# Kernel optimization log

Hardware: AMD Instinct MI355X
Metric: run time of the kernel (lower is better)

The kernel has to match this reference:

```python
import jax, jax.numpy as jnp
import numpy as np

B, C, H, W = 16, 512, 32, 32
GROUPS = 8
EPS = 1e-5


def setup_inputs() -> dict:
    key = jax.random.key(0)
    ks = jax.random.split(key, 7)
    s = 1.0 / np.sqrt(C)
    return {
        "x": jax.random.normal(ks[0], (B, C, H, W), dtype=jnp.float32),
        "gamma": jnp.ones((C,), dtype=jnp.float32),
        "beta": jnp.zeros((C,), dtype=jnp.float32),
        "w_qkv": jax.random.normal(ks[1], (3 * C, C), dtype=jnp.float32) * s,
        "b_qkv": jnp.zeros((3 * C,), dtype=jnp.float32),
        "w_proj": jax.random.normal(ks[2], (C, C), dtype=jnp.float32) * s,
        "b_proj": jnp.zeros((C,), dtype=jnp.float32),
    }


def group_norm(x, gamma, beta):
    b, c, h, w = x.shape
    xg = x.reshape(b, GROUPS, c // GROUPS, h, w)
    mean = xg.mean(axis=(2, 3, 4), keepdims=True)
    var = xg.var(axis=(2, 3, 4), keepdims=True)
    xn = ((xg - mean) * jax.lax.rsqrt(var + EPS)).reshape(b, c, h, w)
    return xn * gamma[None, :, None, None] + beta[None, :, None, None]


def reference(x, gamma, beta, w_qkv, b_qkv, w_proj, b_proj):
    b, c, h, w = x.shape
    n = h * w
    hn = group_norm(x, gamma, beta)
    # 1x1 conv == channel matmul: [3C, C] x [B, C, N] -> [B, 3C, N]
    qkv = jnp.einsum('oc,bcn->bon', w_qkv, hn.reshape(b, c, n)) + b_qkv[None, :, None]
    q, k, v = jnp.split(qkv, 3, axis=1)  # each [B, C, N]
    scale = c ** (-0.5)
    # scores [B, N, N]: q^T k
    attn = jax.nn.softmax(jnp.einsum('bcn,bcm->bnm', q, k) * scale, axis=-1)
    out = jnp.einsum('bnm,bcm->bcn', attn, v)  # [B, C, N]
    proj = jnp.einsum('oc,bcn->bon', w_proj, out) + b_proj[None, :, None]
    return x + proj.reshape(b, c, h, w)
```

## Files before the change

kernel.cpp:

```cpp
#include <hip/hip_runtime.h>


#define BATCH 16
#define CCH 512
#define NSP 1024
#define EPSV 1e-5f
#define BK 32
#define HT 4096

typedef short bf16x8 __attribute__((ext_vector_type(8)));
typedef float f32x4 __attribute__((ext_vector_type(4)));

__device__ __forceinline__ unsigned short f2bf(float f) {
    unsigned int u = __float_as_uint(f);
    u += 0x7FFF + ((u >> 16) & 1);
    return (unsigned short)(u >> 16);
}

__device__ __forceinline__ void glds16(const void* g, void* l) {
    __builtin_amdgcn_global_load_lds(
        (const __attribute__((address_space(1))) unsigned int*)g,
        (__attribute__((address_space(3))) unsigned int*)l, 16, 0, 0);
}

#define XCD_MAP(GX_LOG2, PER, xv, yv, bv)                 \
    const int lin_ = blockIdx.x;                          \
    const int xcd_ = lin_ & 7;                            \
    int slot_ = lin_ >> 3;                                \
    const int hi_ = (slot_ >= (PER)) ? 1 : 0;             \
    const int bv = xcd_ + 8 * hi_;                        \
    slot_ -= hi_ * (PER);                                 \
    const int xv = slot_ & ((1 << (GX_LOG2)) - 1);        \
    const int yv = slot_ >> (GX_LOG2);

__device__ __forceinline__ void gemm128_loop(
    const unsigned short* __restrict__ Ag, const unsigned short* __restrict__ Bg,
    int astr, int bstr, int ktot, short* Al, short* Bl, f32x4* acc) {
    const int t = threadIdx.x;
    const int w = t >> 6, lane = t & 63;
    const int wr = (w >> 1) * 64, wc = (w & 1) * 64;
    const int fr = lane & 15;
    const int fsw = (((lane >> 4) ^ (fr & 3)) * 8);
    const int r0 = t >> 2;
    const int kc = (((t & 3) ^ (r0 & 3)) * 8);
    const unsigned short* Ap0 = Ag + (size_t)r0 * astr + kc;
    const unsigned short* Ap1 = Ag + (size_t)(r0 + 64) * astr + kc;
    const unsigned short* Bp0 = Bg + (size_t)r0 * bstr + kc;
    const unsigned short* Bp1 = Bg + (size_t)(r0 + 64) * bstr + kc;
    short* Alw = Al + w * 512;
    short* Blw = Bl + w * 512;
    for (int k0 = 0; k0 < ktot; k0 += 64) {
        glds16(Ap0 + k0, Alw);
        glds16(Ap1 + k0, Alw + 2048);
        glds16(Ap0 + k0 + 32, Alw + HT);
        glds16(Ap1 + k0 + 32, Alw + HT + 2048);
        glds16(Bp0 + k0, Blw);
        glds16(Bp1 + k0, Blw + 2048);
        glds16(Bp0 + k0 + 32, Blw + HT);
        glds16(Bp1 + k0 + 32, Blw + HT + 2048);
        __syncthreads();
#pragma unroll
        for (int h = 0; h < 2; h++) {
            const short* Ab = Al + h * HT;
            const short* Bb = Bl + h * HT;
            bf16x8 af[4], bfr[4];
#pragma unroll
            for (int mi = 0; mi < 4; mi++)
                af[mi] = *(const bf16x8*)(Ab + (wr + mi * 16 + fr) * BK + fsw);
#pragma unroll
            for (int ni = 0; ni < 4; ni++)
                bfr[ni] = *(const bf16x8*)(Bb + (wc + ni * 16 + fr) * BK + fsw);
#pragma unroll
            for (int mi = 0; mi < 4; mi++)
#pragma unroll
                for (int ni = 0; ni < 4; ni++)
                    acc[mi * 4 + ni] = __builtin_amdgcn_mfma_f32_16x16x32_bf16(
                        af[mi], bfr[ni], acc[mi * 4 + ni], 0, 0, 0);
        }
        __syncthreads();
    }
}

#define EPI_SETUP()                                          \
    const int t = threadIdx.x, lane = t & 63, w = t >> 6;    \
    const int wr = (w >> 1) * 64, wc = (w & 1) * 64;         \
    const int fr = lane & 15, rr0 = (lane >> 4) * 4;

#define ACC_INIT(acc)                                        \
    f32x4 acc[16];                                           \
    _Pragma("unroll") for (int i = 0; i < 16; i++)           \
        acc[i] = (f32x4){0.f, 0.f, 0.f, 0.f};

__global__ __launch_bounds__(256) void setup_k(
    const float* __restrict__ x, float* __restrict__ stats,
    const float* __restrict__ wa, unsigned short* __restrict__ oa, int na4,
    const float* __restrict__ wb, unsigned short* __restrict__ ob, int nb4,
    float* __restrict__ Lsum, const float* __restrict__ bqv,
    unsigned short* __restrict__ wv_t, float* __restrict__ puv) {
    const int t = threadIdx.x;
    const int bx = blockIdx.x;
    __shared__ float rs[4], rq[4];
    __shared__ __align__(16) unsigned short Tt[64 * 72];
    if (bx < 128) {
        const int bg = bx;
        const float4* xp = (const float4*)(x + (size_t)bg * 65536);
        float s = 0.f, q = 0.f;
#pragma unroll
        for (int i = 0; i < 64; i++) {
            float4 v = xp[t + i * 256];
            s += v.x + v.y + v.z + v.w;
            q += v.x * v.x + v.y * v.y + v.z * v.z + v.w * v.w;
        }
#pragma unroll
        for (int off = 32; off; off >>= 1) {
            s += __shfl_down(s, off);
            q += __shfl_down(q, off);
        }
        const int wave = t >> 6, lane = t & 63;
        if (lane == 0) { rs[wave] = s; rq[wave] = q; }
        __syncthreads();
        if (t == 0) {
            float S = rs[0] + rs[1] + rs[2] + rs[3];
            float Q = rq[0] + rq[1] + rq[2] + rq[3];
            const float inv = 1.f / 65536.f;
            float mean = S * inv;
            float var = Q * inv - mean * mean;
            stats[bg * 2] = mean;
            stats[bg * 2 + 1] = rsqrtf(var + EPSV);
        }
    } else if (bx < 896) {
        int i = (bx - 128) * 256 + t;
        const float* src;
        unsigned short* dst;
        int j;
        if (i < na4) { src = wa; dst = oa; j = i; }
        else { j = i - na4; if (j >= nb4) return; src = wb; dst = ob; }
        float4 v = ((const float4*)src)[j];
        ushort4 o;
        o.x = f2bf(v.x); o.y = f2bf(v.y); o.z = f2bf(v.z); o.w = f2bf(v.w);
        ((ushort4*)dst)[j] = o;
    } else if (bx < 912) {
        int i = (bx - 896) * 256 + t;
        ((float4*)Lsum)[i] = (float4){0.f, 0.f, 0.f, 0.f};
    } else if (bx < 976) {
        const int r = bx - 912;
        const float* src = wa + (size_t)2 * 512 * 512;
        const int to = (r >> 3) * 64, tc = (r & 7) * 64;
        const int ol = t >> 2, cs = t & 3;
#pragma unroll
        for (int j = 0; j < 4; j++) {
            float4 v = *(const float4*)(src + (size_t)(to + ol) * 512 + tc + cs * 16 + j * 4);
            int c = cs * 16 + j * 4;
            Tt[(c + 0) * 72 + ol] = f2bf(v.x);
            Tt[(c + 1) * 72 + ol] = f2bf(v.y);
            Tt[(c + 2) * 72 + ol] = f2bf(v.z);
            Tt[(c + 3) * 72 + ol] = f2bf(v.w);
        }
        __syncthreads();
        const int cl = t >> 2, os = t & 3;
        unsigned short* d = wv_t + (size_t)(tc + cl) * 512 + to + os * 16;
        const unsigned short* s2 = Tt + cl * 72 + os * 16;
        *(uint4*)d = *(const uint4*)s2;
        *(uint4*)(d + 8) = *(const uint4*)(s2 + 8);
    } else {
        const int o = (bx - 976) * 256 + t;
        const float* wr_ = wb + (size_t)o * 512;
        const float* bv = bqv + 1024;
        float s = 0.f;
        for (int vv = 0; vv < 512; vv += 4) {
            s += wr_[vv] * bv[vv] + wr_[vv + 1] * bv[vv + 1]
               + wr_[vv + 2] * bv[vv + 2] + wr_[vv + 3] * bv[vv + 3];
        }
        puv[o] = s;
    }
}

__global__ __launch_bounds__(256) void gn_tr_k(
    const float* __restrict__ x, const float* __restrict__ gamma,
    const float* __restrict__ beta, const float* __restrict__ stats,
    unsigned short* __restrict__ hn_t,
    const unsigned short* __restrict__ wp_bf, const unsigned short* __restrict__ wv_t,
    unsigned short* __restrict__ wpv_bf) {
    __shared__ __align__(16) short SM[4 * HT];
    const int lin = blockIdx.x;
    const int t = threadIdx.x;
    if (lin < 16) {
        const int ot = (lin >> 2) * 128, ct2 = (lin & 3) * 128;
        ACC_INIT(acc);
        gemm128_loop(wp_bf + (size_t)ot * 512, wv_t + (size_t)ct2 * 512,
                     512, 512, 512, SM, SM + 2 * HT, acc);
        EPI_SETUP();
#pragma unroll
        for (int ni = 0; ni < 4; ni++) {
            int col = ct2 + wc + ni * 16 + fr;
#pragma unroll
            for (int mi = 0; mi < 4; mi++) {
                int row = ot + wr + mi * 16 + rr0;
#pragma unroll
                for (int r = 0; r < 4; r++)
                    wpv_bf[(size_t)(row + r) * 512 + col] = f2bf(acc[mi * 4 + ni][r]);
            }
        }
        return;
    }
    const int l2 = lin - 16;
    const int nt = l2 & 15, ct = (l2 >> 4) & 7, b = l2 >> 7;
    unsigned short* T = (unsigned short*)SM;
    const float mean = stats[(b * 8 + ct) * 2];
    const float rstd = stats[(b * 8 + ct) * 2 + 1];
    const int cl = t >> 2, nc = t & 3;
    const int c = ct * 64 + cl;
    const float ga = gamma[c] * rstd;
    const float be = beta[c] - mean * ga;
    const float4* xp = (const float4*)(x + ((size_t)b * CCH + c) * NSP + nt * 64);
#pragma unroll
    for (int j = 0; j < 4; j++) {
        float4 v = xp[nc * 4 + j];
        int n = nc * 16 + j * 4;
        T[(n + 0) * 72 + cl] = f2bf(v.x * ga + be);
        T[(n + 1) * 72 + cl] = f2bf(v.y * ga + be);
        T[(n + 2) * 72 + cl] = f2bf(v.z * ga + be);
        T[(n + 3) * 72 + cl] = f2bf(v.w * ga + be);
    }
    __syncthreads();
    const int nl = t >> 2, cc = t & 3;
    unsigned short* dst = hn_t + ((size_t)b * NSP + nt * 64 + nl) * CCH + ct * 64 + cc * 16;
    const unsigned short* src = T + nl * 72 + cc * 16;
    *(uint4*)dst = *(const uint4*)src;
    *(uint4*)(dst + 8) = *(const uint4*)(src + 8);
}

__global__ __launch_bounds__(256) void gemm_qku_k(
    const unsigned short* __restrict__ hn_t, const unsigned short* __restrict__ wq,
    const float* __restrict__ bq, const unsigned short* __restrict__ wpv_bf,
    const float* __restrict__ puv, unsigned short* __restrict__ QKt,
    unsigned short* __restrict__ Ub) {
    __shared__ __align__(16) short Al[2 * HT], Bl[2 * HT];
    XCD_MAP(3, 96, xb, y, b);
    const int ntc = xb * 128;
    ACC_INIT(acc);
    if (y < 8) {
        const int mt = y * 128;
        gemm128_loop(hn_t + ((size_t)b * NSP + mt) * CCH,
                     wq + (size_t)ntc * CCH, CCH, CCH, CCH, Al, Bl, acc);
        unsigned short* Ob = QKt + (size_t)b * NSP * 1024;
        EPI_SETUP();
#pragma unroll
        for (int ni = 0; ni < 4; ni++) {
            int col = ntc + wc + ni * 16 + fr;
            float bias = bq[col];
#pragma unroll
            for (int mi = 0; mi < 4; mi++) {
                int row = mt + wr + mi * 16 + rr0;
#pragma unroll
                for (int r = 0; r < 4; r++)
                    Ob[(size_t)(row + r) * 1024 + col] = f2bf(acc[mi * 4 + ni][r] + bias);
            }
        }
    } else {
        const int mt = (y - 8) * 128;
        gemm128_loop(wpv_bf + (size_t)mt * 512,
                     hn_t + ((size_t)b * NSP + ntc) * CCH, 512, CCH, 512, Al, Bl, acc);
        unsigned short* Ob = Ub + (size_t)b * CCH * NSP;
        EPI_SETUP();
#pragma unroll
        for (int mi = 0; mi < 4; mi++) {
            int row = mt + wr + mi * 16 + rr0;
#pragma unroll
            for (int r = 0; r < 4; r++) {
                float bias = puv[row + r];
#pragma unroll
                for (int ni = 0; ni < 4; ni++) {
                    int col = ntc + wc + ni * 16 + fr;
                    Ob[(size_t)(row + r) * NSP + col] = f2bf(acc[mi * 4 + ni][r] + bias);
                }
            }
        }
    }
}

__global__ __launch_bounds__(256) void gemm_scores_k(
    const unsigned short* __restrict__ QKt, unsigned short* __restrict__ expS,
    float* __restrict__ Lsum) {
    __shared__ __align__(16) short Al[2 * HT], Bl[2 * HT];
    XCD_MAP(3, 64, xb, yb, b);
    const int nt = xb * 128, mt = yb * 128;
    const unsigned short* base = QKt + (size_t)b * NSP * 1024;
    ACC_INIT(acc);
    gemm128_loop(base + (size_t)mt * 1024, base + (size_t)nt * 1024 + 512,
                 1024, 1024, 512, Al, Bl, acc);
    unsigned short* Ob = expS + (size_t)b * NSP * NSP;
    float* Ls = Lsum + (size_t)b * NSP;
    const float scale = 0.044194173824159216f;
    EPI_SETUP();
#pragma unroll
    for (int mi = 0; mi < 4; mi++) {
#pragma unroll
        for (int r = 0; r < 4; r++) {
            const int row = mt + wr + mi * 16 + rr0 + r;
            float rs = 0.f;
#pragma unroll
            for (int ni = 0; ni < 4; ni++) {
                int col = nt + wc + ni * 16 + fr;
                float e = __expf(acc[mi * 4 + ni][r] * scale);
                Ob[(size_t)row * NSP + col] = f2bf(e);
                rs += e;
            }
            rs += __shfl_xor(rs, 1);
            rs += __shfl_xor(rs, 2);
            rs += __shfl_xor(rs, 4);
            rs += __shfl_xor(rs, 8);
            if (fr == 0) atomicAdd(&Ls[row], rs);
        }
    }
}

__global__ __launch_bounds__(256) void gemm_pu_k(
    const unsigned short* __restrict__ Ub, const unsigned short* __restrict__ expS,
    const float* __restrict__ Lsum, const float* __restrict__ x,
    const float* __restrict__ bp, float* __restrict__ out) {
    __shared__ __align__(16) short Al[2 * HT], Bl[2 * HT];
    XCD_MAP(3, 32, xb, yb, b);
    const int nt = xb * 128, ot = yb * 128;
    ACC_INIT(acc);
    gemm128_loop(Ub + ((size_t)b * CCH + ot) * NSP,
                 expS + ((size_t)b * NSP + nt) * NSP, NSP, NSP, NSP, Al, Bl, acc);
    const float* Ls = Lsum + (size_t)b * NSP;
    const size_t bbase = (size_t)b * CCH * NSP;
    EPI_SETUP();
#pragma unroll
    for (int ni = 0; ni < 4; ni++) {
        int col = nt + wc + ni * 16 + fr;
        float invl = __builtin_amdgcn_rcpf(Ls[col]);
#pragma unroll
        for (int mi = 0; mi < 4; mi++) {
            int row = ot + wr + mi * 16 + rr0;
#pragma unroll
            for (int r = 0; r < 4; r++) {
                size_t idx = bbase + (size_t)(row + r) * NSP + col;
                out[idx] = x[idx] + bp[row + r] + acc[mi * 4 + ni][r] * invl;
            }
        }
    }
}

extern "C" void kernel_launch(void* const* d_in, const int* in_sizes, int n_in,
                              void* d_out, int out_size, void* d_ws, size_t ws_size,
                              hipStream_t stream) {
    const float* x = (const float*)d_in[0];
    const float* gamma = (const float*)d_in[1];
    const float* beta = (const float*)d_in[2];
    const float* w_qkv = (const float*)d_in[3];
    const float* b_qkv = (const float*)d_in[4];
    const float* w_proj = (const float*)d_in[5];
    const float* b_proj = (const float*)d_in[6];
    float* out = (float*)d_out;

    char* ws = (char*)d_ws;
    const size_t MB = 1048576;
    const size_t KB = 1024;
    unsigned short* wqkv_bf = (unsigned short*)ws;
    unsigned short* wproj_bf = (unsigned short*)(ws + 1572864);
    float* stats = (float*)(ws + 2 * MB);
    float* Lsum = (float*)(ws + 2 * MB + 64 * KB);
    float* puv = (float*)(ws + 2 * MB + 128 * KB);
    unsigned short* wv_t = (unsigned short*)(ws + 2 * MB + 256 * KB);
    unsigned short* wpv_bf = (unsigned short*)(ws + 3 * MB);
    unsigned short* hn_t = (unsigned short*)(ws + 4 * MB);
    unsigned short* QKt = (unsigned short*)(ws + 24 * MB);
    unsigned short* Ub = (unsigned short*)(ws + 60 * MB);
    unsigned short* expS = (unsigned short*)(ws + 80 * MB);

    setup_k<<<978, 256, 0, stream>>>(x, stats, w_qkv, wqkv_bf, 131072,
                                     w_proj, wproj_bf, 65536, Lsum, b_qkv,
                                     wv_t, puv);
    gn_tr_k<<<2064, 256, 0, stream>>>(x, gamma, beta, stats, hn_t,
                                      wproj_bf, wv_t, wpv_bf);
    gemm_qku_k<<<1536, 256, 0, stream>>>(hn_t, wqkv_bf, b_qkv, wpv_bf, puv,
                                         QKt, Ub);
    gemm_scores_k<<<1024, 256, 0, stream>>>(QKt, expS, Lsum);
    gemm_pu_k<<<512, 256, 0, stream>>>(Ub, expS, Lsum, x, b_proj, out);
}
```

Before: 221.0 us.

## Double-buffer LDS staging in GEMM kernels to overlap loads with MFMA

Adds a double-buffered GEMM main loop that issues global-to-LDS loads for the next 64-wide K slab while computing on the current one, synchronized with explicit vmcnt waits and barriers. The QK/U, scores and PU GEMM kernels switch to it, doubling their LDS footprint to 64 KB per block. The fused weight-product path keeps the single-buffered loop. The aim is to hide global load latency behind MFMA work, at the cost of LDS occupancy and a wasted trailing prefetch that wraps to K offset 0.

New measurement: 204.6 us (median of 3 runs). 1.08x faster.

```diff
diff --git a/kernel.cpp b/kernel.cpp
--- a/kernel.cpp
+++ b/kernel.cpp
@@ -22,6 +22,9 @@
         (const __attribute__((address_space(1))) unsigned int*)g,
         (__attribute__((address_space(3))) unsigned int*)l, 16, 0, 0);
 }
+
+#define MEMF asm volatile("" ::: "memory")
+#define VMW(n) asm volatile("s_waitcnt vmcnt(" #n ")" ::: "memory")
 
 #define XCD_MAP(GX_LOG2, PER, xv, yv, bv)                 \
     const int lin_ = blockIdx.x;                          \
@@ -33,7 +36,75 @@
     const int xv = slot_ & ((1 << (GX_LOG2)) - 1);        \
     const int yv = slot_ >> (GX_LOG2);
 
-__device__ __forceinline__ void gemm128_loop(
+__device__ __forceinline__ void gemm128_dbuf(
+    const unsigned short* __restrict__ Ag, const unsigned short* __restrict__ Bg,
+    int astr, int bstr, int ktot, short* L, f32x4* acc) {
+    const int t = threadIdx.x;
+    const int w = t >> 6, lane = t & 63;
+    const int wr = (w >> 1) * 64, wc = (w & 1) * 64;
+    const int fr = lane & 15;
+    const int fsw = (((lane >> 4) ^ (fr & 3)) * 8);
+    const int r0 = t >> 2;
+    const int kc = (((t & 3) ^ (r0 & 3)) * 8);
+    const unsigned short* Ap0 = Ag + (size_t)r0 * astr + kc;
+    const unsigned short* Ap1 = Ag + (size_t)(r0 + 64) * astr + kc;
+    const unsigned short* Bp0 = Bg + (size_t)r0 * bstr + kc;
+    const unsigned short* Bp1 = Bg + (size_t)(r0 + 64) * bstr + kc;
+    short* lw = L + w * 512;
+
+#define STG(bf, kk) do {                                  \
+    short* aw_ = lw + (bf) * (4 * HT);                    \
+    short* bw_ = aw_ + 2 * HT;                            \
+    glds16(Ap0 + (kk), aw_);                              \
+    glds16(Ap1 + (kk), aw_ + 2048);                       \
+    glds16(Ap0 + (kk) + 32, aw_ + HT);                    \
+    glds16(Ap1 + (kk) + 32, aw_ + HT + 2048);             \
+    glds16(Bp0 + (kk), bw_);                              \
+    glds16(Bp1 + (kk), bw_ + 2048);                       \
+    glds16(Bp0 + (kk) + 32, bw_ + HT);                    \
+    glds16(Bp1 + (kk) + 32, bw_ + HT + 2048);             \
+  } while (0)
+
+#define CMP(bf) do {                                                        \
+    _Pragma("unroll")                                                       \
+    for (int h = 0; h < 2; h++) {                                           \
+        const short* Ab_ = L + (bf) * (4 * HT) + h * HT;                    \
+        const short* Bb_ = Ab_ + 2 * HT;                                    \
+        bf16x8 af[4], bfr[4];                                               \
+        _Pragma("unroll")                                                   \
+        for (int mi = 0; mi < 4; mi++)                                      \
+            af[mi] = *(const bf16x8*)(Ab_ + (wr + mi * 16 + fr) * BK + fsw);\
+        _Pragma("unroll")                                                   \
+        for (int ni = 0; ni < 4; ni++)                                      \
+            bfr[ni] = *(const bf16x8*)(Bb_ + (wc + ni * 16 + fr) * BK + fsw);\
+        _Pragma("unroll")                                                   \
+        for (int mi = 0; mi < 4; mi++)                                      \
+            _Pragma("unroll")                                               \
+            for (int ni = 0; ni < 4; ni++)                                  \
+                acc[mi * 4 + ni] = __builtin_amdgcn_mfma_f32_16x16x32_bf16( \
+                    af[mi], bfr[ni], acc[mi * 4 + ni], 0, 0, 0);            \
+    } } while (0)
+
+    STG(0, 0);
+    for (int k0 = 0; k0 < ktot; k0 += 128) {
+        STG(1, k0 + 64);
+        VMW(8);
+        MEMF; __builtin_amdgcn_s_barrier();
+        CMP(0);
+        MEMF; __builtin_amdgcn_s_barrier();
+        const int kb = (k0 + 128 < ktot) ? k0 + 128 : 0;
+        STG(0, kb);
+        VMW(8);
+        MEMF; __builtin_amdgcn_s_barrier();
+        CMP(1);
+        MEMF; __builtin_amdgcn_s_barrier();
+    }
+    VMW(0);
+#undef STG
+#undef CMP
+}
+
+__device__ __forceinline__ void gemm128_sb(
     const unsigned short* __restrict__ Ag, const unsigned short* __restrict__ Bg,
     int astr, int bstr, int ktot, short* Al, short* Bl, f32x4* acc) {
     const int t = threadIdx.x;
@@ -187,8 +258,8 @@
     if (lin < 16) {
         const int ot = (lin >> 2) * 128, ct2 = (lin & 3) * 128;
         ACC_INIT(acc);
-        gemm128_loop(wp_bf + (size_t)ot * 512, wv_t + (size_t)ct2 * 512,
-                     512, 512, 512, SM, SM + 2 * HT, acc);
+        gemm128_sb(wp_bf + (size_t)ot * 512, wv_t + (size_t)ct2 * 512,
+                   512, 512, 512, SM, SM + 2 * HT, acc);
         EPI_SETUP();
 #pragma unroll
         for (int ni = 0; ni < 4; ni++) {
@@ -235,14 +306,14 @@
     const float* __restrict__ bq, const unsigned short* __restrict__ wpv_bf,
     const float* __restrict__ puv, unsigned short* __restrict__ QKt,
     unsigned short* __restrict__ Ub) {
-    __shared__ __align__(16) short Al[2 * HT], Bl[2 * HT];
+    __shared__ __align__(16) short L[8 * HT];
     XCD_MAP(3, 96, xb, y, b);
     const int ntc = xb * 128;
     ACC_INIT(acc);
     if (y < 8) {
         const int mt = y * 128;
-        gemm128_loop(hn_t + ((size_t)b * NSP + mt) * CCH,
-                     wq + (size_t)ntc * CCH, CCH, CCH, CCH, Al, Bl, acc);
+        gemm128_dbuf(hn_t + ((size_t)b * NSP + mt) * CCH,
+                     wq + (size_t)ntc * CCH, CCH, CCH, CCH, L, acc);
         unsigned short* Ob = QKt + (size_t)b * NSP * 1024;
         EPI_SETUP();
 #pragma unroll
@@ -259,8 +330,8 @@
         }
     } else {
         const int mt = (y - 8) * 128;
-        gemm128_loop(wpv_bf + (size_t)mt * 512,
-                     hn_t + ((size_t)b * NSP + ntc) * CCH, 512, CCH, 512, Al, Bl, acc);
+        gemm128_dbuf(wpv_bf + (size_t)mt * 512,
+                     hn_t + ((size_t)b * NSP + ntc) * CCH, 512, CCH, 512, L, acc);
         unsigned short* Ob = Ub + (size_t)b * CCH * NSP;
         EPI_SETUP();
 #pragma unroll
@@ -282,13 +353,13 @@
 __global__ __launch_bounds__(256) void gemm_scores_k(
     const unsigned short* __restrict__ QKt, unsigned short* __restrict__ expS,
     float* __restrict__ Lsum) {
-    __shared__ __align__(16) short Al[2 * HT], Bl[2 * HT];
+    __shared__ __align__(16) short L[8 * HT];
     XCD_MAP(3, 64, xb, yb, b);
     const int nt = xb * 128, mt = yb * 128;
     const unsigned short* base = QKt + (size_t)b * NSP * 1024;
     ACC_INIT(acc);
-    gemm128_loop(base + (size_t)mt * 1024, base + (size_t)nt * 1024 + 512,
-                 1024, 1024, 512, Al, Bl, acc);
+    gemm128_dbuf(base + (size_t)mt * 1024, base + (size_t)nt * 1024 + 512,
+                 1024, 1024, 512, L, acc);
     unsigned short* Ob = expS + (size_t)b * NSP * NSP;
     float* Ls = Lsum + (size_t)b * NSP;
     const float scale = 0.044194173824159216f;
@@ -319,12 +390,12 @@
     const unsigned short* __restrict__ Ub, const unsigned short* __restrict__ expS,
     const float* __restrict__ Lsum, const float* __restrict__ x,
     const float* __restrict__ bp, float* __restrict__ out) {
-    __shared__ __align__(16) short Al[2 * HT], Bl[2 * HT];
+    __shared__ __align__(16) short L[8 * HT];
     XCD_MAP(3, 32, xb, yb, b);
     const int nt = xb * 128, ot = yb * 128;
     ACC_INIT(acc);
-    gemm128_loop(Ub + ((size_t)b * CCH + ot) * NSP,
-                 expS + ((size_t)b * NSP + nt) * NSP, NSP, NSP, NSP, Al, Bl, acc);
+    gemm128_dbuf(Ub + ((size_t)b * CCH + ot) * NSP,
+                 expS + ((size_t)b * NSP + nt) * NSP, NSP, NSP, NSP, L, acc);
     const float* Ls = Lsum + (size_t)b * NSP;
     const size_t bbase = (size_t)b * CCH * NSP;
     EPI_SETUP();
```
